# Kernel tuning notes

Measured on AMD Instinct MI355X. Metric: run time of the kernel, lower is better.

The kernel has to match this reference:

```python
import jax, jax.numpy as jnp
import numpy as np

B, Din, T, G = 8, 512, 1024, 128
DM, H, L, FF = 512, 8, 2, 2048
MAX_PERIOD = 10000.0


def _ln(x, s, b, eps=1e-5):
    m = x.mean(-1, keepdims=True)
    v = ((x - m) ** 2).mean(-1, keepdims=True)
    return (x - m) * jax.lax.rsqrt(v + eps) * s + b


def _rope(x, pos):
    # x: (B,H,S,Dh), pos: (S,)
    dh = x.shape[-1]
    half = dh // 2
    freqs = 1.0 / (MAX_PERIOD ** (jnp.arange(half, dtype=jnp.float32) / half))
    ang = pos[:, None] * freqs[None, :]              # (S, half)
    cos, sin = jnp.cos(ang), jnp.sin(ang)
    x1, x2 = x[..., :half], x[..., half:]
    return jnp.concatenate([x1 * cos - x2 * sin, x1 * sin + x2 * cos], axis=-1)


def _transformer(x, W_in, b_in, ln1_s, ln1_b, Wq, Wk, Wv, Wo, ls1,
                 ln2_s, ln2_b, W1, b1, W2, b2, ls2, lnf_s, lnf_b, W_out, b_out):
    # x: (B, Din, S) conv layout -> (B, S, DM)
    h = jnp.einsum('bds,de->bse', x, W_in) + b_in
    Bx, S, E = h.shape
    dh = E // H
    pos = jnp.arange(S, dtype=jnp.float32)
    scale = 1.0 / jnp.sqrt(jnp.asarray(dh, h.dtype))
    for l in range(Wq.shape[0]):
        y = _ln(h, ln1_s[l], ln1_b[l])
        q = (y @ Wq[l]).reshape(Bx, S, H, dh).transpose(0, 2, 1, 3)
        k = (y @ Wk[l]).reshape(Bx, S, H, dh).transpose(0, 2, 1, 3)
        v = (y @ Wv[l]).reshape(Bx, S, H, dh).transpose(0, 2, 1, 3)
        q, k = _rope(q, pos), _rope(k, pos)
        att = jax.nn.softmax(jnp.einsum('bhqd,bhkd->bhqk', q, k) * scale, axis=-1)
        o = jnp.einsum('bhqk,bhkd->bhqd', att, v).transpose(0, 2, 1, 3).reshape(Bx, S, E)
        h = h + ls1[l] * (o @ Wo[l])
        y = _ln(h, ln2_s[l], ln2_b[l])
        h = h + ls2[l] * (jax.nn.gelu(y @ W1[l] + b1[l]) @ W2[l] + b2[l])
    h = _ln(h, lnf_s, lnf_b)
    return (h @ W_out + b_out).transpose(0, 2, 1)  # (B, Din, S)


def _forward(features, alignment_matrix, num_segments_per_item, params):
    Bx, D, Tt = features.shape
    Gx = alignment_matrix.shape[1]
    ar_t = jnp.arange(Tt, dtype=jnp.int32)
    ar_g = jnp.arange(Gx, dtype=jnp.int32)
    group_mask = ar_g[None, :] < num_segments_per_item[:, None]          # (B,G)
    group_last = (alignment_matrix * ar_t.astype(features.dtype)).max(axis=2).astype(jnp.int32)  # (B,G)
    valid_last = jnp.where(group_mask, group_last, -1)
    frame_lengths = valid_last.max(axis=1) + 1                            # (B,)
    frame_mask = ar_t[None, :] < frame_lengths[:, None]                   # (B,T)
    last_for_count = jnp.where(group_mask, group_last, Tt + 1)
    num_q_before = jnp.sum(last_for_count[:, :, None] < ar_t[None, None, :], axis=1).astype(jnp.int32)  # (B,T)
    frame_dest = ar_t[None, :] + num_q_before                             # (B,T)
    query_dest = group_last + ar_g[None, :] + 1                           # (B,G)
    # mean-pooled query init
    summed = jnp.einsum('bgt,bdt->bgd', alignment_matrix, features)
    counts = jnp.maximum(alignment_matrix.sum(axis=2), 1.0)
    queries = (summed / counts[..., None]).transpose(0, 2, 1)             # (B,D,G)
    source_seq = jnp.concatenate([features, queries], axis=2)             # (B,D,T+G)
    dest = jnp.concatenate([frame_dest, query_dest], axis=1)              # (B,T+G)
    smask = jnp.concatenate([frame_mask, group_mask], axis=1)
    dest_m = jnp.where(smask, dest, Tt + Gx)
    perm = jnp.argsort(dest_m, axis=1)                                    # (B,T+G)
    interleaved = jnp.take_along_axis(source_seq, perm[:, None, :], axis=2)
    tout = _transformer(interleaved, *params)                             # (B,D,T+G)
    inv_perm = jnp.argsort(perm, axis=1)
    qpos = inv_perm[:, Tt:]                                               # (B,G)
    agg = jnp.take_along_axis(tout, qpos[:, None, :], axis=2)             # (B,D,G)
    return jnp.where(group_mask[:, None, :], agg, 0.0)


def setup_inputs() -> dict:
    key = jax.random.key(0)
    ks = jax.random.split(key, 8)
    rng = np.random.default_rng(0)
    align = np.zeros((B, G, T), np.float32)
    num_seg = np.zeros((B,), np.int32)
    for b in range(B):
        n = int(rng.integers(G // 2, G + 1))
        cuts = np.sort(rng.choice(np.arange(1, T), n - 1, replace=False))
        gid = np.searchsorted(cuts, np.arange(T), side='right')
        align[b, gid, np.arange(T)] = 1.0
        num_seg[b] = n
    s = 0.02
    return {
        'features': jax.random.normal(ks[0], (B, Din, T), jnp.float32),
        'alignment_matrix': jnp.asarray(align),
        'num_segments_per_item': jnp.asarray(num_seg),
        'W_in': jax.random.normal(ks[1], (Din, DM), jnp.float32) * s,
        'b_in': jnp.zeros((DM,), jnp.float32),
        'ln1_s': jnp.ones((L, DM), jnp.float32), 'ln1_b': jnp.zeros((L, DM), jnp.float32),
        'Wq': jax.random.normal(ks[2], (L, DM, DM), jnp.float32) * s,
        'Wk': jax.random.normal(ks[3], (L, DM, DM), jnp.float32) * s,
        'Wv': jax.random.normal(ks[4], (L, DM, DM), jnp.float32) * s,
        'Wo': jax.random.normal(ks[5], (L, DM, DM), jnp.float32) * s,
        'ls1': 0.01 * jnp.ones((L, DM), jnp.float32),
        'ln2_s': jnp.ones((L, DM), jnp.float32), 'ln2_b': jnp.zeros((L, DM), jnp.float32),
        'W1': jax.random.normal(ks[6], (L, DM, FF), jnp.float32) * s,
        'b1': jnp.zeros((L, FF), jnp.float32),
        'W2': jax.random.normal(ks[7], (L, FF, DM), jnp.float32) * s,
        'b2': jnp.zeros((L, DM), jnp.float32),
        'ls2': 0.01 * jnp.ones((L, DM), jnp.float32),
        'lnf_s': jnp.ones((DM,), jnp.float32), 'lnf_b': jnp.zeros((DM,), jnp.float32),
        'W_out': jax.random.normal(jax.random.fold_in(key, 9), (DM, Din), jnp.float32) * s,
        'b_out': jnp.zeros((Din,), jnp.float32),
    }


def reference(features, alignment_matrix, num_segments_per_item, W_in, b_in, ln1_s, ln1_b,
              Wq, Wk, Wv, Wo, ls1, ln2_s, ln2_b, W1, b1, W2, b2, ls2, lnf_s, lnf_b, W_out, b_out):
    params = (W_in, b_in, ln1_s, ln1_b, Wq, Wk, Wv, Wo, ls1,
              ln2_s, ln2_b, W1, b1, W2, b2, ls2, lnf_s, lnf_b, W_out, b_out)
    return _forward(features, alignment_matrix, num_segments_per_item, params)
```

## Files before the change

kernel.cpp:

```cpp
#include <hip/hip_runtime.h>
#include <hip/hip_bf16.h>
#include <math.h>

#define NB   8
#define NT   1024
#define NG   128
#define NS   1152
#define NDIN 512
#define NDM  512
#define NH   8
#define NDH  64
#define NFF  2048
#define NL   2

typedef __attribute__((ext_vector_type(4))) float  floatx4;
typedef __attribute__((ext_vector_type(8))) short  shortx8;

__device__ __forceinline__ float gelu_f(float x) {
    float u = 1.5957691216057308f * (x + 0.044715f * x * x * x);
    return x / (1.0f + __expf(-u));
}

__device__ __forceinline__ void gload_lds16(const void* g, void* l) {
    __builtin_amdgcn_global_load_lds((const __attribute__((address_space(1))) unsigned int*)g,
                                     (__attribute__((address_space(3))) unsigned int*)l, 16, 0, 0);
}

__device__ __forceinline__ short f2bfs(float x) {
    __hip_bfloat16 h = __float2bfloat16(x);
    return *(short*)&h;
}
__device__ __forceinline__ unsigned pack_bf2_rz(float a, float b) {
    unsigned au = *(unsigned*)&a, bu = *(unsigned*)&b;
    return (au >> 16) | (bu & 0xFFFF0000u);
}

__device__ __forceinline__ void swzxy(int& bx, int& by, int gx, int gy) {
    const int nwg = gx * gy;
    int flat = by * gx + bx;
    if ((nwg & 7) == 0) flat = (flat & 7) * (nwg >> 3) + (flat >> 3);
    bx = flat % gx; by = flat / gx;
}

__device__ __forceinline__ void wtile(const float* __restrict__ src,
        __hip_bfloat16* __restrict__ dst, int K, int N, int i, int tid, short tile[32][33])
{
    const int gx = N / 32;
    const int n0 = (i % gx) * 32;
    const int k0 = (i / gx) * 32;
    {
        const int r = tid >> 3, c4 = (tid & 7) * 4;
        float4 v = *(const float4*)&src[(size_t)(k0 + r) * N + n0 + c4];
        tile[c4 + 0][r] = f2bfs(v.x);
        tile[c4 + 1][r] = f2bfs(v.y);
        tile[c4 + 2][r] = f2bfs(v.z);
        tile[c4 + 3][r] = f2bfs(v.w);
    }
    __syncthreads();
    {
        const int r = tid >> 3, c4 = (tid & 7) * 4;
        short* dp = (short*)dst + (size_t)(n0 + r) * K + k0 + c4;
        short4 v;
        v.x = tile[r][c4 + 0]; v.y = tile[r][c4 + 1];
        v.z = tile[r][c4 + 2]; v.w = tile[r][c4 + 3];
        *(short4*)dp = v;
    }
}

__global__ __launch_bounds__(256) void prep0_k(
        float2* __restrict__ tab,
        const float* __restrict__ features, float* __restrict__ featT,
        const float* W_in, const float* Wq, const float* Wk, const float* Wv,
        const float* Wo, const float* W1, const float* W2, const float* W_out,
        __hip_bfloat16* w_inT, __hip_bfloat16* wqkvT0, __hip_bfloat16* wqkvT1,
        __hip_bfloat16* woT0, __hip_bfloat16* woT1,
        __hip_bfloat16* w1T0, __hip_bfloat16* w1T1,
        __hip_bfloat16* w2T0, __hip_bfloat16* w2T1, __hip_bfloat16* woutT)
{
    __shared__ __align__(16) char smem[32 * 33 * 4];
    const int tid = threadIdx.x;
    const int blk = blockIdx.x;
    if (blk < 144) {
        const int idx = blk * 256 + tid;
        const int s = idx >> 5, i = idx & 31;
        const float fr = __expf(-(float)i * 0.28782313662425576f);
        const float ang = (float)s * fr;
        tab[idx] = make_float2(cosf(ang), sinf(ang));
    } else if (blk < 144 + 4096) {
        float (*tile)[33] = (float(*)[33])smem;
        const int v = blk - 144;
        const int t0 = (v & 31) * 32;
        const int d0 = ((v >> 5) & 15) * 32;
        const int b  = v >> 9;
        const int r = tid >> 3, c4 = (tid & 7) * 4;
        {
            float4 w = *(const float4*)&features[((size_t)(b * NDIN + d0 + r)) * NT + t0 + c4];
            tile[c4 + 0][r] = w.x; tile[c4 + 1][r] = w.y;
            tile[c4 + 2][r] = w.z; tile[c4 + 3][r] = w.w;
        }
        __syncthreads();
        {
            float4 w;
            w.x = tile[r][c4 + 0]; w.y = tile[r][c4 + 1];
            w.z = tile[r][c4 + 2]; w.w = tile[r][c4 + 3];
            *(float4*)&featT[((size_t)(b * NT + t0 + r)) * NDIN + d0 + c4] = w;
        }
    } else {
        short (*tile)[33] = (short(*)[33])smem;
        const int i = blk - (144 + 4096);
        const float* src; __hip_bfloat16* dst; int K, N, ti;
        if (i < 256) { src = W_in; dst = w_inT; K = 512; N = 512; ti = i; }
        else if (i < 6400) {
            int r = i - 256;
            const int l = r / 3072; r -= l * 3072;
            const size_t o5 = (size_t)l * 262144, o2 = (size_t)l * 1048576;
            if (r < 256)       { src = Wq + o5; dst = (l ? wqkvT1 : wqkvT0);          K = 512;  N = 512;  ti = r; }
            else if (r < 512)  { src = Wk + o5; dst = (l ? wqkvT1 : wqkvT0) + 262144; K = 512;  N = 512;  ti = r - 256; }
            else if (r < 768)  { src = Wv + o5; dst = (l ? wqkvT1 : wqkvT0) + 524288; K = 512;  N = 512;  ti = r - 512; }
            else if (r < 1024) { src = Wo + o5; dst = (l ? woT1 : woT0);              K = 512;  N = 512;  ti = r - 768; }
            else if (r < 2048) { src = W1 + o2; dst = (l ? w1T1 : w1T0);              K = 512;  N = 2048; ti = r - 1024; }
            else               { src = W2 + o2; dst = (l ? w2T1 : w2T0);              K = 2048; N = 512;  ti = r - 2048; }
        }
        else { src = W_out; dst = woutT; K = 512; N = 512; ti = i - 6400; }
        wtile(src, dst, K, N, ti, tid, tile);
    }
}

__global__ __launch_bounds__(256) void pool_k(const float* __restrict__ align,
        const float* __restrict__ featT, int* __restrict__ glast,
        float* __restrict__ queries)
{
    __shared__ float redf[256];
    __shared__ int   redi[256];
    __shared__ float aw[NT];
    const int bg = blockIdx.x;
    const int b = bg >> 7;
    const int tid = threadIdx.x;
    const float* arow = align + (size_t)bg * NT;
    float cnt = 0.f, last = 0.f;
    int tmin = NT;
    for (int t = tid; t < NT; t += 256) {
        float a = arow[t];
        cnt += a;
        last = fmaxf(last, a * (float)t);
        if (a > 0.f) tmin = min(tmin, t);
    }
    redf[tid] = cnt; __syncthreads();
    for (int s = 128; s > 0; s >>= 1) { if (tid < s) redf[tid] += redf[tid + s]; __syncthreads(); }
    float c = redf[0]; __syncthreads();
    redf[tid] = last; __syncthreads();
    for (int s = 128; s > 0; s >>= 1) { if (tid < s) redf[tid] = fmaxf(redf[tid], redf[tid + s]); __syncthreads(); }
    float l = redf[0];
    redi[tid] = tmin; __syncthreads();
    for (int s = 128; s > 0; s >>= 1) { if (tid < s) redi[tid] = min(redi[tid], redi[tid + s]); __syncthreads(); }
    const int t0 = redi[0];
    const int t1 = (int)l;
    if (tid == 0) glast[bg] = t1;
    __syncthreads();
    for (int t = t0 + tid; t <= t1; t += 256) aw[t - t0] = arow[t];
    __syncthreads();
    const float invc = 1.0f / fmaxf(c, 1.0f);
    const float* fT = featT + (size_t)b * NT * NDIN;
    for (int d = tid; d < NDIN; d += 256) {
        float s = 0.f;
        for (int t = t0; t <= t1; ++t) s += aw[t - t0] * fT[(size_t)t * NDIN + d];
        queries[(size_t)bg * NDIN + d] = s * invc;
    }
}

__global__ __launch_bounds__(256) void rank_k(const int* __restrict__ glast,
        const int* __restrict__ nsegp, int* __restrict__ perm, int* __restrict__ qpos)
{
    __shared__ int dm[NS];
    __shared__ int gl[NG];
    const int b = blockIdx.y;
    const int tid = threadIdx.x;
    const int j = blockIdx.x * 256 + tid;
    if (tid < NG) gl[tid] = glast[b * NG + tid];
    const int ns = nsegp[b];
    __syncthreads();
    for (int jj = tid; jj < NS; jj += 256) {
        int d;
        if (jj < NT) {
            int t = jj, nq = 0, flen = 0;
            for (int g = 0; g < ns; ++g) {
                flen = max(flen, gl[g] + 1);
                nq += (gl[g] < t) ? 1 : 0;
            }
            d = (t < flen) ? (t + nq) : NS;
        } else {
            int g = jj - NT;
            d = (g < ns) ? (gl[g] + g + 1) : NS;
        }
        dm[jj] = d;
    }
    __syncthreads();
    if (j < NS) {
        const int my = dm[j];
        int r = 0;
        for (int t = 0; t < NS; ++t) {
            int v2 = dm[t];
            r += (v2 < my || (v2 == my && t < j)) ? 1 : 0;
        }
        perm[b * NS + r] = j;
        if (j >= NT) qpos[b * NG + (j - NT)] = r;
    }
}

__global__ __launch_bounds__(256) void buildx_k(const float* __restrict__ featT,
        const float* __restrict__ queries, const int* __restrict__ perm,
        __hip_bfloat16* __restrict__ X)
{
    const int idx = blockIdx.x * 256 + threadIdx.x;
    if (idx >= NB * NS * (NDIN / 4)) return;
    const int dq = idx & 127;
    const int p = (idx >> 7) % NS;
    const int b = idx / (NS * 128);
    const int j = perm[b * NS + p];
    const float4* src = (j < NT)
        ? (const float4*)&featT[((size_t)(b * NT + j)) * NDIN]
        : (const float4*)&queries[((size_t)(b * NG + (j - NT))) * NDIN];
    float4 v = src[dq];
    short4 o;
    o.x = f2bfs(v.x); o.y = f2bfs(v.y); o.z = f2bfs(v.z); o.w = f2bfs(v.w);
    *(short4*)((short*)X + ((size_t)(b * NS + p)) * NDIN + dq * 4) = o;
}

__global__ __launch_bounds__(256) void bgemmw1_k(const __hip_bfloat16* __restrict__ A,
        const __hip_bfloat16* __restrict__ Bt, __hip_bfloat16* __restrict__ Cout,
        const float* __restrict__ bias, int M, int N, int K)
{
    __shared__ __align__(16) short SM[4][128 * 32];
    const int tid = threadIdx.x;
    const int wave = tid >> 6, lane = tid & 63;
    const int quad = lane >> 4, l16 = lane & 15;
    const int wm = wave >> 1, wn = wave & 1;
    int bx = blockIdx.x, by = blockIdx.y;
    swzxy(bx, by, gridDim.x, gridDim.y);
    const size_t bm = (size_t)by * 128, bn = (size_t)bx * 128;
    const int sw = (l16 >> 1) & 3;
    const short* Ag = (const short*)A;
    const short* Bg = (const short*)Bt;
    const int lrow = lane >> 2;
    const int lchunk = (lane & 3) ^ ((lane >> 3) & 3);
    const int rS = wave * 32;

    floatx4 acc[4][4];
#pragma unroll
    for (int i = 0; i < 4; ++i)
#pragma unroll
        for (int j = 0; j < 4; ++j) acc[i][j] = (floatx4){0.f, 0.f, 0.f, 0.f};

    {
        const size_t ra = (bm + rS + lrow) * (size_t)K + lchunk * 8;
        const size_t rb = (bn + rS + lrow) * (size_t)K + lchunk * 8;
        gload_lds16(Ag + ra,                    &SM[0][rS * 32]);
        gload_lds16(Ag + ra + 16 * (size_t)K,   &SM[0][(rS + 16) * 32]);
        gload_lds16(Bg + rb,                    &SM[2][rS * 32]);
        gload_lds16(Bg + rb + 16 * (size_t)K,   &SM[2][(rS + 16) * 32]);
    }
    __syncthreads();
    int cur = 0;
    for (int k0 = 0; k0 < K; k0 += 32) {
        if (k0 + 32 < K) {
            const int nx = cur ^ 1;
            const size_t ra = (bm + rS + lrow) * (size_t)K + (k0 + 32) + lchunk * 8;
            const size_t rb = (bn + rS + lrow) * (size_t)K + (k0 + 32) + lchunk * 8;
            gload_lds16(Ag + ra,                  &SM[nx][rS * 32]);
            gload_lds16(Ag + ra + 16 * (size_t)K, &SM[nx][(rS + 16) * 32]);
            gload_lds16(Bg + rb,                  &SM[2 + nx][rS * 32]);
            gload_lds16(Bg + rb + 16 * (size_t)K, &SM[2 + nx][(rS + 16) * 32]);
        }
        shortx8 af[4], bf[4];
#pragma unroll
        for (int t = 0; t < 4; ++t) {
            af[t] = *(const shortx8*)&SM[cur][(wm * 64 + t * 16 + l16) * 32 + ((quad ^ sw) * 8)];
            bf[t] = *(const shortx8*)&SM[2 + cur][(wn * 64 + t * 16 + l16) * 32 + ((quad ^ sw) * 8)];
        }
#pragma unroll
        for (int mt = 0; mt < 4; ++mt)
#pragma unroll
            for (int nt = 0; nt < 4; ++nt)
                acc[mt][nt] = __builtin_amdgcn_mfma_f32_16x16x32_bf16(af[mt], bf[nt], acc[mt][nt], 0, 0, 0);
        __syncthreads();
        cur ^= 1;
    }
    const size_t mbase = bm + wm * 64;
    const size_t nbase = bn + wn * 64;
    short* ep = &SM[wave][0];
#pragma unroll
    for (int nt = 0; nt < 4; ++nt) {
        const size_t n = nbase + nt * 16 + l16;
        const float bz = bias[n];
        const int col = nt * 16 + l16;
#pragma unroll
        for (int mt = 0; mt < 4; ++mt)
#pragma unroll
            for (int r = 0; r < 4; ++r) {
                const int rl = mt * 16 + quad * 4 + r;
                float e = gelu_f(acc[mt][nt][r] + bz);
                ep[rl * 64 + (((col >> 3) ^ (rl & 7)) * 8) + (col & 7)] = f2bfs(e);
            }
    }
    __asm__ __volatile__("" ::: "memory");
#pragma unroll
    for (int c2 = 0; c2 < 8; ++c2) {
        const int rl = c2 * 8 + (lane >> 3);
        const int cc = lane & 7;
        shortx8 v = *(const shortx8*)&ep[rl * 64 + ((cc ^ (rl & 7)) * 8)];
        *(shortx8*)((short*)Cout + (mbase + rl) * N + nbase + cc * 8) = v;
    }
}

__global__ __launch_bounds__(256) void bgemmqkv_k(const __hip_bfloat16* __restrict__ A,
        const __hip_bfloat16* __restrict__ Bt, __hip_bfloat16* __restrict__ qh,
        __hip_bfloat16* __restrict__ kh, __hip_bfloat16* __restrict__ vT,
        const float2* __restrict__ tab)
{
    __shared__ __align__(16) short SM[4][128 * 32];
    const int tid = threadIdx.x;
    const int wave = tid >> 6, lane = tid & 63;
    const int quad = lane >> 4, l16 = lane & 15;
    const int wm = wave >> 1, wn = wave & 1;
    int bx = blockIdx.x, by = blockIdx.y;
    swzxy(bx, by, gridDim.x, gridDim.y);
    const size_t bm = (size_t)by * 128, bn = (size_t)bx * 128;
    const int sw = (l16 >> 1) & 3;
    const int K = 512;
    const short* Ag = (const short*)A;
    const short* Bg = (const short*)Bt;
    const int lrow = lane >> 2;
    const int lchunk = (lane & 3) ^ ((lane >> 3) & 3);
    const int rS = wave * 32;

    floatx4 acc[4][4];
#pragma unroll
    for (int i = 0; i < 4; ++i)
#pragma unroll
        for (int j = 0; j < 4; ++j) acc[i][j] = (floatx4){0.f, 0.f, 0.f, 0.f};

    {
        const size_t ra = (bm + rS + lrow) * (size_t)K + lchunk * 8;
        const size_t rb = (bn + rS + lrow) * (size_t)K + lchunk * 8;
        gload_lds16(Ag + ra,                  &SM[0][rS * 32]);
        gload_lds16(Ag + ra + 16 * (size_t)K, &SM[0][(rS + 16) * 32]);
        gload_lds16(Bg + rb,                  &SM[2][rS * 32]);
        gload_lds16(Bg + rb + 16 * (size_t)K, &SM[2][(rS + 16) * 32]);
    }
    __syncthreads();
    int cur = 0;
    for (int k0 = 0; k0 < K; k0 += 32) {
        if (k0 + 32 < K) {
            const int nx = cur ^ 1;
            const size_t ra = (bm + rS + lrow) * (size_t)K + (k0 + 32) + lchunk * 8;
            const size_t rb = (bn + rS + lrow) * (size_t)K + (k0 + 32) + lchunk * 8;
            gload_lds16(Ag + ra,                  &SM[nx][rS * 32]);
            gload_lds16(Ag + ra + 16 * (size_t)K, &SM[nx][(rS + 16) * 32]);
            gload_lds16(Bg + rb,                  &SM[2 + nx][rS * 32]);
            gload_lds16(Bg + rb + 16 * (size_t)K, &SM[2 + nx][(rS + 16) * 32]);
        }
        shortx8 af[4], bf[4];
#pragma unroll
        for (int t = 0; t < 4; ++t) {
            af[t] = *(const shortx8*)&SM[cur][(wm * 64 + t * 16 + l16) * 32 + ((quad ^ sw) * 8)];
            bf[t] = *(const shortx8*)&SM[2 + cur][(wn * 64 + t * 16 + l16) * 32 + ((quad ^ sw) * 8)];
        }
#pragma unroll
        for (int mt = 0; mt < 4; ++mt)
#pragma unroll
            for (int nt = 0; nt < 4; ++nt)
                acc[mt][nt] = __builtin_amdgcn_mfma_f32_16x16x32_bf16(af[mt], bf[nt], acc[mt][nt], 0, 0, 0);
        __syncthreads();
        cur ^= 1;
    }
    short* ep = &SM[wave][0];
    const int bidx = (int)(bm / NS);
    const int sbase = (int)(bm - (size_t)bidx * NS) + wm * 64;
    const int region = (int)(bn >> 9);
    if (region < 2) {
        const float qsc = region ? 1.0f : 0.18033688011112043f;
        const int h = (int)((((int)bn & 511) + wn * 64) >> 6);
#pragma unroll
        for (int nt = 0; nt < 2; ++nt) {
            const int d1 = nt * 16 + l16, d2 = d1 + 32;
            const float2* tp = tab + d1;
#pragma unroll
            for (int mt = 0; mt < 4; ++mt)
#pragma unroll
                for (int r = 0; r < 4; ++r) {
                    const int sl = mt * 16 + quad * 4 + r;
                    const int s = sbase + sl;
                    float x1 = acc[mt][nt][r], x2 = acc[mt][nt + 2][r];
                    float2 cs = tp[s * 32];
                    ep[sl * 64 + (((d1 >> 3) ^ (sl & 7)) * 8) + (d1 & 7)] = f2bfs(qsc * (x1 * cs.x - x2 * cs.y));
                    ep[sl * 64 + (((d2 >> 3) ^ (sl & 7)) * 8) + (d2 & 7)] = f2bfs(qsc * (x1 * cs.y + x2 * cs.x));
                }
        }
        __asm__ __volatile__("" ::: "memory");
        short* dst = (short*)(region ? kh : qh) + ((size_t)(bidx * NH + h)) * NS * NDH;
#pragma unroll
        for (int c2 = 0; c2 < 8; ++c2) {
            const int sl = c2 * 8 + (lane >> 3);
            const int cc = lane & 7;
            shortx8 v = *(const shortx8*)&ep[sl * 64 + ((cc ^ (sl & 7)) * 8)];
            *(shortx8*)(dst + (size_t)(sbase + sl) * NDH + cc * 8) = v;
        }
    } else {
        const int base = (int)(bn - 1024) + wn * 64;
        const int h = base >> 6;
#pragma unroll
        for (int nt = 0; nt < 4; ++nt) {
            const int dl = nt * 16 + l16;
#pragma unroll
            for (int mt = 0; mt < 4; ++mt)
#pragma unroll
                for (int r = 0; r < 4; ++r) {
                    const int sl = mt * 16 + quad * 4 + r;
                    ep[dl * 64 + (((sl >> 3) ^ (dl & 7)) * 8) + (sl & 7)] = f2bfs(acc[mt][nt][r]);
                }
        }
        __asm__ __volatile__("" ::: "memory");
        short* vp = (short*)vT + ((size_t)(bidx * NH + h)) * NDH * NS;
#pragma unroll
        for (int c2 = 0; c2 < 8; ++c2) {
            const int dl = c2 * 8 + (lane >> 3);
            const int cc = lane & 7;
            shortx8 v = *(const shortx8*)&ep[dl * 64 + ((cc ^ (dl & 7)) * 8)];
            *(shortx8*)(vp + (size_t)dl * NS + sbase + cc * 8) = v;
        }
    }
}

template <int EPI>
__global__ __launch_bounds__(256) void bgemm64_k(const __hip_bfloat16* __restrict__ A,
        const __hip_bfloat16* __restrict__ Bt, void* __restrict__ Cout,
        const float* __restrict__ bias, const float* __restrict__ ls,
        const float* __restrict__ res, const int* __restrict__ nsegp, int M, int N, int K)
{
    __shared__ __align__(16) short As[2][64 * 32];
    __shared__ __align__(16) short Bs[2][128 * 32];
    const int tid = threadIdx.x;
    const int wave = tid >> 6, lane = tid & 63;
    const int quad = lane >> 4, l16 = lane & 15;
    const int wm = wave >> 1, wn = wave & 1;
    int bx = blockIdx.x, by = blockIdx.y;
    swzxy(bx, by, gridDim.x, gridDim.y);
    const size_t bm = (size_t)by * 64, bn = (size_t)bx * 128;
    const int sw = (l16 >> 1) & 3;
    const short* Ag = (const short*)A;
    const short* Bg = (const short*)Bt;
    const int lrow = lane >> 2;
    const int lchunk = (lane & 3) ^ ((lane >> 3) & 3);
    const int rA = wave * 16, rB = wave * 32;

    floatx4 acc[2][4];
#pragma unroll
    for (int i = 0; i < 2; ++i)
#pragma unroll
        for (int j = 0; j < 4; ++j) acc[i][j] = (floatx4){0.f, 0.f, 0.f, 0.f};

    {
        const size_t ra = (bm + rA + lrow) * (size_t)K + lchunk * 8;
        const size_t rb = (bn + rB + lrow) * (size_t)K + lchunk * 8;
        gload_lds16(Ag + ra,                  &As[0][rA * 32]);
        gload_lds16(Bg + rb,                  &Bs[0][rB * 32]);
        gload_lds16(Bg + rb + 16 * (size_t)K, &Bs[0][(rB + 16) * 32]);
    }
    __syncthreads();
    int cur = 0;
    for (int k0 = 0; k0 < K; k0 += 32) {
        if (k0 + 32 < K) {
            const int nx = cur ^ 1;
            const size_t ra = (bm + rA + lrow) * (size_t)K + (k0 + 32) + lchunk * 8;
            const size_t rb = (bn + rB + lrow) * (size_t)K + (k0 + 32) + lchunk * 8;
            gload_lds16(Ag + ra,                  &As[nx][rA * 32]);
            gload_lds16(Bg + rb,                  &Bs[nx][rB * 32]);
            gload_lds16(Bg + rb + 16 * (size_t)K, &Bs[nx][(rB + 16) * 32]);
        }
        shortx8 af[2], bf[4];
#pragma unroll
        for (int t = 0; t < 2; ++t)
            af[t] = *(const shortx8*)&As[cur][(wm * 32 + t * 16 + l16) * 32 + ((quad ^ sw) * 8)];
#pragma unroll
        for (int t = 0; t < 4; ++t)
            bf[t] = *(const shortx8*)&Bs[cur][(wn * 64 + t * 16 + l16) * 32 + ((quad ^ sw) * 8)];
#pragma unroll
        for (int mt = 0; mt < 2; ++mt)
#pragma unroll
            for (int nt = 0; nt < 4; ++nt)
                acc[mt][nt] = __builtin_amdgcn_mfma_f32_16x16x32_bf16(af[mt], bf[nt], acc[mt][nt], 0, 0, 0);
        __syncthreads();
        cur ^= 1;
    }
    const size_t mbase = bm + wm * 32;
    const size_t nbase = bn + wn * 64;
#pragma unroll
    for (int nt = 0; nt < 4; ++nt) {
        const size_t n = nbase + nt * 16 + l16;
        const float bz = bias ? bias[n] : 0.f;
        const float lz = (EPI == 2) ? ls[n] : 0.f;
#pragma unroll
        for (int mt = 0; mt < 2; ++mt) {
#pragma unroll
            for (int r = 0; r < 4; ++r) {
                const size_t m = mbase + mt * 16 + quad * 4 + r;
                float e = acc[mt][nt][r] + bz;
                if (EPI == 4) {
                    const int b = (int)(m >> 7), g = (int)(m & 127);
                    float val = (g < nsegp[b]) ? e : 0.0f;
                    ((float*)Cout)[(size_t)b * (NDIN * NG) + n * NG + g] = val;
                } else {
                    const size_t off = m * N + n;
                    if (EPI == 2) e = res[off] + lz * e;
                    ((float*)Cout)[off] = e;
                }
            }
        }
    }
}

__global__ __launch_bounds__(256) void lnw_k(const float* __restrict__ in,
        __hip_bfloat16* __restrict__ out, const float* __restrict__ gam, const float* __restrict__ bet)
{
    const int r = blockIdx.x * 4 + (threadIdx.x >> 6);
    const int t = threadIdx.x & 63;
    const float4* xp = (const float4*)(in + (size_t)r * NDM);
    float4 a = xp[t * 2], b4 = xp[t * 2 + 1];
    float s = a.x + a.y + a.z + a.w + b4.x + b4.y + b4.z + b4.w;
#pragma unroll
    for (int o = 1; o < 64; o <<= 1) s += __shfl_xor(s, o);
    const float mean = s * (1.0f / NDM);
    float dx[8] = {a.x - mean, a.y - mean, a.z - mean, a.w - mean,
                   b4.x - mean, b4.y - mean, b4.z - mean, b4.w - mean};
    float v = 0.f;
#pragma unroll
    for (int i = 0; i < 8; ++i) v += dx[i] * dx[i];
#pragma unroll
    for (int o = 1; o < 64; o <<= 1) v += __shfl_xor(v, o);
    const float inv = rsqrtf(v * (1.0f / NDM) + 1e-5f);
    const float4* gp = (const float4*)gam;
    const float4* bp = (const float4*)bet;
    float4 g0 = gp[t * 2], g1 = gp[t * 2 + 1], q0 = bp[t * 2], q1 = bp[t * 2 + 1];
    shortx8 o8;
    o8[0] = f2bfs(dx[0] * inv * g0.x + q0.x);
    o8[1] = f2bfs(dx[1] * inv * g0.y + q0.y);
    o8[2] = f2bfs(dx[2] * inv * g0.z + q0.z);
    o8[3] = f2bfs(dx[3] * inv * g0.w + q0.w);
    o8[4] = f2bfs(dx[4] * inv * g1.x + q1.x);
    o8[5] = f2bfs(dx[5] * inv * g1.y + q1.y);
    o8[6] = f2bfs(dx[6] * inv * g1.z + q1.z);
    o8[7] = f2bfs(dx[7] * inv * g1.w + q1.w);
    *(shortx8*)((short*)out + (size_t)r * NDM + t * 8) = o8;
}

__global__ __launch_bounds__(64) void lnwg_k(const float* __restrict__ h,
        __hip_bfloat16* __restrict__ out, const float* __restrict__ gam, const float* __restrict__ bet,
        const int* __restrict__ qpos)
{
    const int r = blockIdx.x, t = threadIdx.x;
    const int b = r >> 7;
    const int src = qpos[r];
    const float4* xp = (const float4*)(h + ((size_t)(b * NS + src)) * NDM);
    float4 a = xp[t * 2], b4 = xp[t * 2 + 1];
    float s = a.x + a.y + a.z + a.w + b4.x + b4.y + b4.z + b4.w;
#pragma unroll
    for (int o = 1; o < 64; o <<= 1) s += __shfl_xor(s, o);
    const float mean = s * (1.0f / NDM);
    float dx[8] = {a.x - mean, a.y - mean, a.z - mean, a.w - mean,
                   b4.x - mean, b4.y - mean, b4.z - mean, b4.w - mean};
    float v = 0.f;
#pragma unroll
    for (int i = 0; i < 8; ++i) v += dx[i] * dx[i];
#pragma unroll
    for (int o = 1; o < 64; o <<= 1) v += __shfl_xor(v, o);
    const float inv = rsqrtf(v * (1.0f / NDM) + 1e-5f);
    const float4* gp = (const float4*)gam;
    const float4* bp = (const float4*)bet;
    float4 g0 = gp[t * 2], g1 = gp[t * 2 + 1], q0 = bp[t * 2], q1 = bp[t * 2 + 1];
    shortx8 o8;
    o8[0] = f2bfs(dx[0] * inv * g0.x + q0.x);
    o8[1] = f2bfs(dx[1] * inv * g0.y + q0.y);
    o8[2] = f2bfs(dx[2] * inv * g0.z + q0.z);
    o8[3] = f2bfs(dx[3] * inv * g0.w + q0.w);
    o8[4] = f2bfs(dx[4] * inv * g1.x + q1.x);
    o8[5] = f2bfs(dx[5] * inv * g1.y + q1.y);
    o8[6] = f2bfs(dx[6] * inv * g1.z + q1.z);
    o8[7] = f2bfs(dx[7] * inv * g1.w + q1.w);
    *(shortx8*)((short*)out + (size_t)r * NDM + t * 8) = o8;
}

#define FKT 64
#define FKP 68
#define NTL (NS / FKT)
__global__ __launch_bounds__(256) void fattn_k(const __hip_bfloat16* __restrict__ qb,
        const __hip_bfloat16* __restrict__ kb, const __hip_bfloat16* __restrict__ vbT,
        __hip_bfloat16* __restrict__ o)
{
    __shared__ __align__(16) short Ks[FKT * FKP];
    __shared__ __align__(16) short Vt[NDH * FKP];
    __shared__ __align__(16) short Pl[64 * FKP];
    const int tid = threadIdx.x;
    const int wave = tid >> 6, lane = tid & 63;
    const int quad = lane >> 4, l16 = lane & 15;
    const int L = blockIdx.x;
    const int xcd = L & 7, sl = L >> 3;
    const int bh = (xcd << 3) | (sl & 7);
    const int q0 = (sl >> 3) * 64;
    const int bb = bh >> 3, hh = bh & 7;
    const short* qbase = (const short*)qb + (size_t)bh * NS * NDH;
    const short* kbase = (const short*)kb + (size_t)bh * NS * NDH;
    const short* vbase = (const short*)vbT + (size_t)bh * NDH * NS;

    shortx8 Qf0, Qf1;
    {
        const short* qp = qbase + (size_t)(q0 + wave * 16 + l16) * NDH + quad * 8;
        Qf0 = *(const shortx8*)qp;
        Qf1 = *(const shortx8*)(qp + 32);
    }
    shortx8 Of;
#pragma unroll
    for (int i = 0; i < 8; ++i) Of[i] = 0x3F80;

    floatx4 Oacc[4];
#pragma unroll
    for (int i = 0; i < 4; ++i) Oacc[i] = (floatx4){0.f, 0.f, 0.f, 0.f};
    floatx4 Oacc5 = (floatx4){0.f, 0.f, 0.f, 0.f};

    const int sr = tid >> 2, sc = (tid & 3) * 16;
    const int prow = wave * 16 + l16;
    const short* kg = kbase + (size_t)sr * NDH + sc;
    const short* vg = vbase + (size_t)sr * NS + sc;

    shortx8 pk0 = *(const shortx8*)kg, pk1 = *(const shortx8*)(kg + 8);
    shortx8 pv0 = *(const shortx8*)vg, pv1 = *(const shortx8*)(vg + 8);
    *(shortx8*)&Ks[sr * FKP + sc]     = pk0;
    *(shortx8*)&Ks[sr * FKP + sc + 8] = pk1;
    kg += FKT * NDH;
    pk0 = *(const shortx8*)kg; pk1 = *(const shortx8*)(kg + 8);
    __syncthreads();

    floatx4 S[4], Sn[4];
#pragma unroll
    for (int kbk = 0; kbk < 4; ++kbk) {
        shortx8 kf0 = *(const shortx8*)&Ks[(kbk * 16 + l16) * FKP + quad * 8];
        shortx8 kf1 = *(const shortx8*)&Ks[(kbk * 16 + l16) * FKP + 32 + quad * 8];
        floatx4 sa = (floatx4){0.f, 0.f, 0.f, 0.f};
        sa = __builtin_amdgcn_mfma_f32_16x16x32_bf16(kf0, Qf0, sa, 0, 0, 0);
        sa = __builtin_amdgcn_mfma_f32_16x16x32_bf16(kf1, Qf1, sa, 0, 0, 0);
        S[kbk] = sa;
    }

#pragma unroll 2
    for (int t = 0; t < NTL; ++t) {
        __syncthreads();
        if (t + 1 < NTL) {
            *(shortx8*)&Ks[sr * FKP + sc]     = pk0;
            *(shortx8*)&Ks[sr * FKP + sc + 8] = pk1;
        }
        *(shortx8*)&Vt[sr * FKP + sc]     = pv0;
        *(shortx8*)&Vt[sr * FKP + sc + 8] = pv1;
        __syncthreads();
        if (t + 1 < NTL) {
            if (t + 2 < NTL) {
                kg += FKT * NDH;
                pk0 = *(const shortx8*)kg; pk1 = *(const shortx8*)(kg + 8);
            }
            vg += FKT;
            pv0 = *(const shortx8*)vg; pv1 = *(const shortx8*)(vg + 8);
            __builtin_amdgcn_s_setprio(1);
#pragma unroll
            for (int kbk = 0; kbk < 4; ++kbk) {
                shortx8 kf0 = *(const shortx8*)&Ks[(kbk * 16 + l16) * FKP + quad * 8];
                shortx8 kf1 = *(const shortx8*)&Ks[(kbk * 16 + l16) * FKP + 32 + quad * 8];
                floatx4 sa = (floatx4){0.f, 0.f, 0.f, 0.f};
                sa = __builtin_amdgcn_mfma_f32_16x16x32_bf16(kf0, Qf0, sa, 0, 0, 0);
                sa = __builtin_amdgcn_mfma_f32_16x16x32_bf16(kf1, Qf1, sa, 0, 0, 0);
                Sn[kbk] = sa;
            }
            __builtin_amdgcn_s_setprio(0);
        }
#pragma unroll
        for (int kbk = 0; kbk < 4; ++kbk) {
            uint2 u;
            u.x = pack_bf2_rz(exp2f(S[kbk][0]), exp2f(S[kbk][1]));
            u.y = pack_bf2_rz(exp2f(S[kbk][2]), exp2f(S[kbk][3]));
            *(uint2*)&Pl[prow * FKP + kbk * 16 + quad * 4] = u;
        }
        __asm__ __volatile__("" ::: "memory");
        shortx8 Pf0 = *(const shortx8*)&Pl[prow * FKP + quad * 8];
        shortx8 Pf1 = *(const shortx8*)&Pl[prow * FKP + 32 + quad * 8];
        __builtin_amdgcn_s_setprio(1);
#pragma unroll
        for (int ct = 0; ct < 4; ++ct) {
            shortx8 vf0 = *(const shortx8*)&Vt[(ct * 16 + l16) * FKP + quad * 8];
            shortx8 vf1 = *(const shortx8*)&Vt[(ct * 16 + l16) * FKP + 32 + quad * 8];
            Oacc[ct] = __builtin_amdgcn_mfma_f32_16x16x32_bf16(Pf0, vf0, Oacc[ct], 0, 0, 0);
            Oacc[ct] = __builtin_amdgcn_mfma_f32_16x16x32_bf16(Pf1, vf1, Oacc[ct], 0, 0, 0);
        }
        Oacc5 = __builtin_amdgcn_mfma_f32_16x16x32_bf16(Pf0, Of, Oacc5, 0, 0, 0);
        Oacc5 = __builtin_amdgcn_mfma_f32_16x16x32_bf16(Pf1, Of, Oacc5, 0, 0, 0);
        __builtin_amdgcn_s_setprio(0);
#pragma unroll
        for (int i = 0; i < 4; ++i) S[i] = Sn[i];
    }
#pragma unroll
    for (int i = 0; i < 4; ++i) {
        const float inv = 1.0f / Oacc5[i];
        const int row = q0 + wave * 16 + quad * 4 + i;
        __hip_bfloat16* op = o + ((size_t)(bb * NS + row)) * NDM + hh * NDH + l16;
        op[0]  = __float2bfloat16(Oacc[0][i] * inv);
        op[16] = __float2bfloat16(Oacc[1][i] * inv);
        op[32] = __float2bfloat16(Oacc[2][i] * inv);
        op[48] = __float2bfloat16(Oacc[3][i] * inv);
    }
}

extern "C" void kernel_launch(void* const* d_in, const int* in_sizes, int n_in,
                              void* d_out, int out_size, void* d_ws, size_t ws_size,
                              hipStream_t stream) {
    const float* features = (const float*)d_in[0];
    const float* align    = (const float*)d_in[1];
    const int*   nseg     = (const int*)d_in[2];
    const float* W_in  = (const float*)d_in[3];
    const float* b_in  = (const float*)d_in[4];
    const float* ln1_s = (const float*)d_in[5];
    const float* ln1_b = (const float*)d_in[6];
    const float* Wq = (const float*)d_in[7];
    const float* Wk = (const float*)d_in[8];
    const float* Wv = (const float*)d_in[9];
    const float* Wo = (const float*)d_in[10];
    const float* ls1   = (const float*)d_in[11];
    const float* ln2_s = (const float*)d_in[12];
    const float* ln2_b = (const float*)d_in[13];
    const float* W1 = (const float*)d_in[14];
    const float* b1 = (const float*)d_in[15];
    const float* W2 = (const float*)d_in[16];
    const float* b2 = (const float*)d_in[17];
    const float* ls2   = (const float*)d_in[18];
    const float* lnf_s = (const float*)d_in[19];
    const float* lnf_b = (const float*)d_in[20];
    const float* W_out = (const float*)d_in[21];
    const float* b_out = (const float*)d_in[22];

    const size_t SZ_BSD = (size_t)NB * NS * NDM;

    float* p = (float*)d_ws;
    __hip_bfloat16* w_inT  = (__hip_bfloat16*)p;
    __hip_bfloat16* wqkvT0 = w_inT + 512 * 512;
    __hip_bfloat16* wqkvT1 = wqkvT0 + 1536 * 512;
    __hip_bfloat16* woT0   = wqkvT1 + 1536 * 512;
    __hip_bfloat16* woT1   = woT0 + 512 * 512;
    __hip_bfloat16* w1T0   = woT1 + 512 * 512;
    __hip_bfloat16* w1T1   = w1T0 + 2048 * 512;
    __hip_bfloat16* w2T0   = w1T1 + 2048 * 512;
    __hip_bfloat16* w2T1   = w2T0 + 512 * 2048;
    __hip_bfloat16* woutT  = w2T1 + 512 * 2048;
    int* glast = (int*)(woutT + 512 * 512);
    int* perm  = glast + NB * NG;
    int* qpos  = perm + NB * NS;
    float2* ropetab = (float2*)(qpos + NB * NG);
    p = (float*)(ropetab + NS * 32);

    float* featT = p; p += (size_t)NB * NT * NDIN;
    float* hbuf = p; p += SZ_BSD;
    __hip_bfloat16* ybuf = (__hip_bfloat16*)p;  p += SZ_BSD / 2;
    __hip_bfloat16* obuf = (__hip_bfloat16*)p;  p += SZ_BSD / 2;
    __hip_bfloat16* ubuf = (__hip_bfloat16*)p;  p += SZ_BSD * 2;
    __hip_bfloat16* xin  = (__hip_bfloat16*)p;  p += SZ_BSD / 2;
    float* quer = p; p += (size_t)NB * NG * NDIN;
    __hip_bfloat16* hq = (__hip_bfloat16*)p; p += (size_t)NB * NG * NDM / 2;
    const size_t needed = (size_t)((char*)p - (char*)d_ws);
    if (ws_size < needed) return;

    __hip_bfloat16* qh = ubuf;
    __hip_bfloat16* kh = ubuf + SZ_BSD;
    __hip_bfloat16* vT = xin;

    prep0_k<<<144 + 4096 + 6656, 256, 0, stream>>>(ropetab, features, featT,
            W_in, Wq, Wk, Wv, Wo, W1, W2, W_out,
            w_inT, wqkvT0, wqkvT1, woT0, woT1, w1T0, w1T1, w2T0, w2T1, woutT);
    pool_k<<<NB * NG, 256, 0, stream>>>(align, featT, glast, quer);
    rank_k<<<dim3((NS + 255) / 256, NB), 256, 0, stream>>>(glast, nseg, perm, qpos);
    buildx_k<<<(NB * NS * (NDIN / 4) + 255) / 256, 256, 0, stream>>>(featT, quer, perm, xin);

    const int M = NB * NS;
    bgemm64_k<0><<<dim3(NDM / 128, M / 64), 256, 0, stream>>>(xin, w_inT, hbuf, b_in, nullptr, nullptr, nullptr, M, NDM, NDIN);

    for (int l = 0; l < NL; ++l) {
        __hip_bfloat16* wqkvT = (l ? wqkvT1 : wqkvT0);
        __hip_bfloat16* woT   = (l ? woT1 : woT0);
        __hip_bfloat16* w1T   = (l ? w1T1 : w1T0);
        __hip_bfloat16* w2T   = (l ? w2T1 : w2T0);

        lnw_k<<<M / 4, 256, 0, stream>>>(hbuf, ybuf, ln1_s + l * NDM, ln1_b + l * NDM);
        bgemmqkv_k<<<dim3(1536 / 128, M / 128), 256, 0, stream>>>(ybuf, wqkvT, qh, kh, vT, ropetab);
        fattn_k<<<(NS / 64) * NH * NB, 256, 0, stream>>>(qh, kh, vT, obuf);
        bgemm64_k<2><<<dim3(NDM / 128, M / 64), 256, 0, stream>>>(obuf, woT, hbuf, nullptr, ls1 + l * NDM, hbuf, nullptr, M, NDM, NDM);
        lnw_k<<<M / 4, 256, 0, stream>>>(hbuf, ybuf, ln2_s + l * NDM, ln2_b + l * NDM);
        bgemmw1_k<<<dim3(NFF / 128, M / 128), 256, 0, stream>>>(ybuf, w1T, ubuf, b1 + l * NFF, M, NFF, NDM);
        bgemm64_k<2><<<dim3(NDM / 128, M / 64), 256, 0, stream>>>(ubuf, w2T, hbuf, b2 + l * NDM, ls2 + l * NDM, hbuf, nullptr, M, NDM, NFF);
    }

    lnwg_k<<<NB * NG, 64, 0, stream>>>(hbuf, hq, lnf_s, lnf_b, qpos);
    bgemm64_k<4><<<dim3(NDIN / 128, (NB * NG) / 64), 256, 0, stream>>>(hq, woutT, d_out, b_out, nullptr, nullptr, nseg, NB * NG, NDIN, NDM);
}
```

Baseline: 602.1 us.

## Load K and V fragments directly from global memory in flash attention

```diff
diff --git a/kernel.cpp b/kernel.cpp
--- a/kernel.cpp
+++ b/kernel.cpp
@@ -596,8 +596,6 @@
         const __hip_bfloat16* __restrict__ kb, const __hip_bfloat16* __restrict__ vbT,
         __hip_bfloat16* __restrict__ o)
 {
-    __shared__ __align__(16) short Ks[FKT * FKP];
-    __shared__ __align__(16) short Vt[NDH * FKP];
     __shared__ __align__(16) short Pl[64 * FKP];
     const int tid = threadIdx.x;
     const int wave = tid >> 6, lane = tid & 63;
@@ -626,58 +624,32 @@
     for (int i = 0; i < 4; ++i) Oacc[i] = (floatx4){0.f, 0.f, 0.f, 0.f};
     floatx4 Oacc5 = (floatx4){0.f, 0.f, 0.f, 0.f};
 
-    const int sr = tid >> 2, sc = (tid & 3) * 16;
     const int prow = wave * 16 + l16;
-    const short* kg = kbase + (size_t)sr * NDH + sc;
-    const short* vg = vbase + (size_t)sr * NS + sc;
-
-    shortx8 pk0 = *(const shortx8*)kg, pk1 = *(const shortx8*)(kg + 8);
-    shortx8 pv0 = *(const shortx8*)vg, pv1 = *(const shortx8*)(vg + 8);
-    *(shortx8*)&Ks[sr * FKP + sc]     = pk0;
-    *(shortx8*)&Ks[sr * FKP + sc + 8] = pk1;
-    kg += FKT * NDH;
-    pk0 = *(const shortx8*)kg; pk1 = *(const shortx8*)(kg + 8);
-    __syncthreads();
-
-    floatx4 S[4], Sn[4];
-#pragma unroll
-    for (int kbk = 0; kbk < 4; ++kbk) {
-        shortx8 kf0 = *(const shortx8*)&Ks[(kbk * 16 + l16) * FKP + quad * 8];
-        shortx8 kf1 = *(const shortx8*)&Ks[(kbk * 16 + l16) * FKP + 32 + quad * 8];
-        floatx4 sa = (floatx4){0.f, 0.f, 0.f, 0.f};
-        sa = __builtin_amdgcn_mfma_f32_16x16x32_bf16(kf0, Qf0, sa, 0, 0, 0);
-        sa = __builtin_amdgcn_mfma_f32_16x16x32_bf16(kf1, Qf1, sa, 0, 0, 0);
-        S[kbk] = sa;
-    }
-
-#pragma unroll 2
+    const short* kp = kbase + (size_t)l16 * NDH + quad * 8;
+    const short* vp = vbase + (size_t)l16 * NS + quad * 8;
+
     for (int t = 0; t < NTL; ++t) {
-        __syncthreads();
-        if (t + 1 < NTL) {
-            *(shortx8*)&Ks[sr * FKP + sc]     = pk0;
-            *(shortx8*)&Ks[sr * FKP + sc + 8] = pk1;
-        }
-        *(shortx8*)&Vt[sr * FKP + sc]     = pv0;
-        *(shortx8*)&Vt[sr * FKP + sc + 8] = pv1;
-        __syncthreads();
-        if (t + 1 < NTL) {
-            if (t + 2 < NTL) {
-                kg += FKT * NDH;
-                pk0 = *(const shortx8*)kg; pk1 = *(const shortx8*)(kg + 8);
-            }
-            vg += FKT;
-            pv0 = *(const shortx8*)vg; pv1 = *(const shortx8*)(vg + 8);
-            __builtin_amdgcn_s_setprio(1);
-#pragma unroll
-            for (int kbk = 0; kbk < 4; ++kbk) {
-                shortx8 kf0 = *(const shortx8*)&Ks[(kbk * 16 + l16) * FKP + quad * 8];
-                shortx8 kf1 = *(const shortx8*)&Ks[(kbk * 16 + l16) * FKP + 32 + quad * 8];
-                floatx4 sa = (floatx4){0.f, 0.f, 0.f, 0.f};
-                sa = __builtin_amdgcn_mfma_f32_16x16x32_bf16(kf0, Qf0, sa, 0, 0, 0);
-                sa = __builtin_amdgcn_mfma_f32_16x16x32_bf16(kf1, Qf1, sa, 0, 0, 0);
-                Sn[kbk] = sa;
-            }
-            __builtin_amdgcn_s_setprio(0);
+        shortx8 kf0[4], kf1[4];
+#pragma unroll
+        for (int kbk = 0; kbk < 4; ++kbk) {
+            const short* kq = kp + (size_t)(t * FKT + kbk * 16) * NDH;
+            kf0[kbk] = *(const shortx8*)kq;
+            kf1[kbk] = *(const shortx8*)(kq + 32);
+        }
+        floatx4 S[4];
+#pragma unroll
+        for (int kbk = 0; kbk < 4; ++kbk) {
+            floatx4 sa = (floatx4){0.f, 0.f, 0.f, 0.f};
+            sa = __builtin_amdgcn_mfma_f32_16x16x32_bf16(kf0[kbk], Qf0, sa, 0, 0, 0);
+            sa = __builtin_amdgcn_mfma_f32_16x16x32_bf16(kf1[kbk], Qf1, sa, 0, 0, 0);
+            S[kbk] = sa;
+        }
+        shortx8 vf0[4], vf1[4];
+#pragma unroll
+        for (int ct = 0; ct < 4; ++ct) {
+            const short* vq = vp + (size_t)(ct * 16) * NS + t * FKT;
+            vf0[ct] = *(const shortx8*)vq;
+            vf1[ct] = *(const shortx8*)(vq + 32);
         }
 #pragma unroll
         for (int kbk = 0; kbk < 4; ++kbk) {
@@ -692,16 +664,12 @@
         __builtin_amdgcn_s_setprio(1);
 #pragma unroll
         for (int ct = 0; ct < 4; ++ct) {
-            shortx8 vf0 = *(const shortx8*)&Vt[(ct * 16 + l16) * FKP + quad * 8];
-            shortx8 vf1 = *(const shortx8*)&Vt[(ct * 16 + l16) * FKP + 32 + quad * 8];
-            Oacc[ct] = __builtin_amdgcn_mfma_f32_16x16x32_bf16(Pf0, vf0, Oacc[ct], 0, 0, 0);
-            Oacc[ct] = __builtin_amdgcn_mfma_f32_16x16x32_bf16(Pf1, vf1, Oacc[ct], 0, 0, 0);
+            Oacc[ct] = __builtin_amdgcn_mfma_f32_16x16x32_bf16(Pf0, vf0[ct], Oacc[ct], 0, 0, 0);
+            Oacc[ct] = __builtin_amdgcn_mfma_f32_16x16x32_bf16(Pf1, vf1[ct], Oacc[ct], 0, 0, 0);
         }
         Oacc5 = __builtin_amdgcn_mfma_f32_16x16x32_bf16(Pf0, Of, Oacc5, 0, 0, 0);
         Oacc5 = __builtin_amdgcn_mfma_f32_16x16x32_bf16(Pf1, Of, Oacc5, 0, 0, 0);
         __builtin_amdgcn_s_setprio(0);
-#pragma unroll
-        for (int i = 0; i < 4; ++i) S[i] = Sn[i];
     }
 #pragma unroll
     for (int i = 0; i < 4; ++i) {
```

Result: slower. 822.5 us (+36.6%).
